# Performance work log

Measured on AMD Instinct MI355X. Metric: run time of the kernel, lower is better.

## Reference

```python
import jax, jax.numpy as jnp
import numpy as np

B, S, E, H = 1, 4096, 768, 12
D = E // H  # head_dim = 64


def setup_inputs() -> dict:
    key = jax.random.key(0)
    ks = jax.random.split(key, 6)
    scale = 0.02
    x = jax.random.normal(ks[0], (B, S, E), dtype=jnp.float32)
    Wq = jax.random.normal(ks[1], (E, E), dtype=jnp.float32) * scale
    Wk = jax.random.normal(ks[2], (E, E), dtype=jnp.float32) * scale
    Wv = jax.random.normal(ks[3], (E, E), dtype=jnp.float32) * scale
    Wo = jax.random.normal(ks[4], (E, E), dtype=jnp.float32) * scale
    bo = jax.random.normal(ks[5], (E,), dtype=jnp.float32) * scale
    mask = jnp.tril(jnp.ones((S, S), dtype=bool))[None, None]  # [1,1,S,S] causal
    return {"x": x, "Wq": Wq, "Wk": Wk, "Wv": Wv, "Wo": Wo, "bo": bo, "mask": mask}


def reference(x, Wq, Wk, Wv, Wo, bo, mask):
    # projections (torch Linear: y = x @ W.T; here W stored as [E,E] applied as x@W)
    q = jnp.einsum('bse,ef->bsf', x, Wq).reshape(B, S, H, D).transpose(0, 2, 1, 3)
    k = jnp.einsum('bse,ef->bsf', x, Wk).reshape(B, S, H, D).transpose(0, 2, 1, 3)
    v = jnp.einsum('bse,ef->bsf', x, Wv).reshape(B, S, H, D).transpose(0, 2, 1, 3)
    scores = jnp.einsum('bhqd,bhkd->bhqk', q, k) / jnp.sqrt(jnp.float32(D))
    scores = jnp.where(mask, scores, -jnp.inf)
    attn = jax.nn.softmax(scores, axis=-1)  # dropout p=0 -> identity
    ctx = jnp.einsum('bhqk,bhkd->bhqd', attn, v)
    ctx = ctx.transpose(0, 2, 1, 3).reshape(B, S, E)
    return jnp.einsum('bse,ef->bsf', ctx, Wo) + bo
```

## Files before the change

### kernel.cpp

```cpp
#include <hip/hip_runtime.h>
#include <math.h>

#define S 4096
#define E 768
#define H 12
#define Dh 64
#define SCALE2 0.1803368801111204f

typedef short short8 __attribute__((ext_vector_type(8)));
typedef float floatx4 __attribute__((ext_vector_type(4)));

__device__ __forceinline__ unsigned short f2bf(float f) {
    union { float f; unsigned int i; } c; c.f = f;
    unsigned int i = c.i;
    return (unsigned short)((i + 0x7fffu + ((i >> 16) & 1u)) >> 16);
}

__device__ __forceinline__ unsigned int pk_bf16(float lo, float hi) {
#if __has_builtin(__builtin_amdgcn_cvt_pk_bf16_f32)
    typedef __bf16 bf16x2 __attribute__((ext_vector_type(2)));
    union { bf16x2 v; unsigned int u; } c;
    c.v = __builtin_amdgcn_cvt_pk_bf16_f32(lo, hi);
    return c.u;
#else
    union { float f; unsigned int i; } a, b; a.f = lo; b.f = hi;
    return ((a.i + 0x8000u) >> 16) | ((b.i + 0x8000u) & 0xFFFF0000u);
#endif
}

__device__ __forceinline__ unsigned int scale_pk(unsigned int u, float s) {
    union { unsigned int i; float f; } lo, hi;
    lo.i = u << 16; hi.i = u & 0xffff0000u;
    return pk_bf16(lo.f * s, hi.f * s);
}

__device__ __forceinline__ void pk_atomic_add_bf16(unsigned short* addr, unsigned int bits) {
    unsigned long long a = (unsigned long long)addr;
    asm volatile("global_atomic_pk_add_bf16 %0, %1, off" :: "v"(a), "v"(bits) : "memory");
}

__device__ __forceinline__ void gload_lds16(const unsigned short* g, unsigned short* l) {
    __builtin_amdgcn_global_load_lds(
        (const __attribute__((address_space(1))) unsigned int*)g,
        (__attribute__((address_space(3))) unsigned int*)l, 16, 0, 0);
}

__global__ __launch_bounds__(256)
void prep_kernel(const float* __restrict__ x, unsigned short* __restrict__ xb,
                 const float* __restrict__ s0, const float* __restrict__ s1,
                 const float* __restrict__ s2, const float* __restrict__ s3,
                 unsigned short* __restrict__ d0, unsigned short* __restrict__ d1,
                 unsigned short* __restrict__ d2, unsigned short* __restrict__ d3,
                 char* __restrict__ zbase) {
    __shared__ unsigned short tile[32][33];
    const int b = blockIdx.x;
    const int tid = threadIdx.x;
    if (b < 2304) {
        int z = b / 576, rem = b - z * 576;
        int bx = rem % 24, by = rem / 24;
        const float* src = (z == 0) ? s0 : (z == 1) ? s1 : (z == 2) ? s2 : s3;
        unsigned short* dst = (z == 0) ? d0 : (z == 1) ? d1 : (z == 2) ? d2 : d3;
        int tx = tid & 31, ty = tid >> 5;
        int xcol = bx * 32 + tx;
        int y0 = by * 32;
        for (int j = ty; j < 32; j += 8)
            tile[j][tx] = f2bf(src[(size_t)(y0 + j) * E + xcol]);
        __syncthreads();
        int x2 = y0 + tx;
        int y2 = bx * 32;
        for (int j = ty; j < 32; j += 8)
            dst[(size_t)(y2 + j) * E + x2] = tile[tx][j];
    } else if (b < 3840) {
        int i = ((b - 2304) * 256 + tid) * 8;
        float4 f0 = *reinterpret_cast<const float4*>(x + i);
        float4 f1 = *reinterpret_cast<const float4*>(x + i + 4);
        unsigned short u[8];
        u[0]=f2bf(f0.x); u[1]=f2bf(f0.y); u[2]=f2bf(f0.z); u[3]=f2bf(f0.w);
        u[4]=f2bf(f1.x); u[5]=f2bf(f1.y); u[6]=f2bf(f1.z); u[7]=f2bf(f1.w);
        *reinterpret_cast<uint4*>(xb + i) = *reinterpret_cast<uint4*>(u);
    } else {
        size_t i = (size_t)(b - 3840) * 16384 + (size_t)tid * 64;
        uint4 z4 = make_uint4(0u, 0u, 0u, 0u);
        *reinterpret_cast<uint4*>(zbase + i)      = z4;
        *reinterpret_cast<uint4*>(zbase + i + 16) = z4;
        *reinterpret_cast<uint4*>(zbase + i + 32) = z4;
        *reinterpret_cast<uint4*>(zbase + i + 48) = z4;
    }
}

__global__ __launch_bounds__(256)
void gemm_qkv(const unsigned short* __restrict__ A,
              const unsigned short* __restrict__ BT,
              unsigned short* __restrict__ Qb, unsigned short* __restrict__ Kb,
              unsigned short* __restrict__ VTb) {
    __shared__ unsigned short Asm[128 * 64];
    __shared__ unsigned short Bsm[128 * 64];
    const int tid  = threadIdx.x;
    const int wave = tid >> 6, lane = tid & 63;
    const int quad = lane >> 4, l16 = lane & 15;
    const int lrow = lane >> 3, lchunk = lane & 7;
    const int bb = blockIdx.x;
    const int xcd = bb & 7, j = bb >> 3;
    const int mt = (xcd >> 1) * 8 + (j & 7);
    const int nt = (xcd & 1) * 9 + (j >> 3);
    const int n0 = nt * 128;
    const int m0 = mt * 128;
    const int aw = wave >> 1, bw = wave & 1;

    floatx4 acc[4][4];
    #pragma unroll
    for (int at = 0; at < 4; at++)
        #pragma unroll
        for (int ct = 0; ct < 4; ct++)
            #pragma unroll
            for (int r = 0; r < 4; r++) acc[at][ct][r] = 0.f;

    for (int k0 = 0; k0 < E; k0 += 64) {
        #pragma unroll
        for (int i = 0; i < 4; i++) {
            int rbase = wave * 32 + i * 8;
            int row   = rbase + lrow;
            int gc    = lchunk ^ (row & 7);
            gload_lds16(&A [(size_t)(m0 + row) * E + k0 + gc * 8], &Asm[rbase * 64]);
            gload_lds16(&BT[(size_t)(n0 + row) * E + k0 + gc * 8], &Bsm[rbase * 64]);
        }
        __syncthreads();
        #pragma unroll
        for (int kk = 0; kk < 2; kk++) {
            const int g = kk * 4 + quad;
            short8 af[4], bfr[4];
            #pragma unroll
            for (int t = 0; t < 4; t++) {
                int ar = aw * 64 + t * 16 + l16;
                af[t]  = *reinterpret_cast<const short8*>(&Asm[ar * 64 + (g ^ (ar & 7)) * 8]);
                int br = bw * 64 + t * 16 + l16;
                bfr[t] = *reinterpret_cast<const short8*>(&Bsm[br * 64 + (g ^ (br & 7)) * 8]);
            }
            #pragma unroll
            for (int at = 0; at < 4; at++)
                #pragma unroll
                for (int ct = 0; ct < 4; ct++)
                    acc[at][ct] = __builtin_amdgcn_mfma_f32_16x16x32_bf16(af[at], bfr[ct], acc[at][ct], 0, 0, 0);
        }
        __syncthreads();
    }

    const int sec = n0 / 768;
    const int nb  = n0 - sec * 768 + bw * 64;
    if (sec == 2) {
        #pragma unroll
        for (int at = 0; at < 4; at++)
            #pragma unroll
            for (int ct = 0; ct < 4; ct++) {
                int nsec = nb + ct * 16 + l16, hh = nsec >> 6, d = nsec & 63;
                int s0i = m0 + aw * 64 + at * 16 + quad * 4;
                uint2 w2;
                w2.x = pk_bf16(acc[at][ct][0], acc[at][ct][1]);
                w2.y = pk_bf16(acc[at][ct][2], acc[at][ct][3]);
                *reinterpret_cast<uint2*>(&VTb[(size_t)hh * Dh * S + (size_t)d * S + s0i]) = w2;
            }
    } else {
        #pragma unroll
        for (int at = 0; at < 4; at++)
            #pragma unroll
            for (int ct = 0; ct < 4; ct++) {
                int nsec = nb + ct * 16 + l16, hh = nsec >> 6, d = nsec & 63;
                #pragma unroll
                for (int r = 0; r < 4; r++) {
                    int s = m0 + aw * 64 + at * 16 + quad * 4 + r;
                    float v = acc[at][ct][r];
                    if (sec == 0) Qb[(size_t)hh * S * Dh + (size_t)s * Dh + d] = f2bf(v * SCALE2);
                    else          Kb[(size_t)hh * S * Dh + (size_t)s * Dh + d] = f2bf(v);
                }
            }
    }
}

__global__ __launch_bounds__(256)
void gemm_out(const unsigned short* __restrict__ ctxp,
              const unsigned short* __restrict__ BT,
              const float* __restrict__ lsumf,
              float* __restrict__ outp, const float* __restrict__ bias) {
    __shared__ unsigned short Asm[128 * 64];
    __shared__ unsigned short Bsm[64 * 64];
    const int tid  = threadIdx.x;
    const int wave = tid >> 6, lane = tid & 63;
    const int quad = lane >> 4, l16 = lane & 15;
    const int lrow = lane >> 3, lchunk = lane & 7;
    const int bb = blockIdx.x;
    const int xcd = bb & 7, j = bb >> 3;
    const int mt = (xcd >> 1) * 8 + (j & 7);
    const int nt = (xcd & 1) * 6 + (j >> 3);
    const int n0 = nt * 64;
    const int m0 = mt * 128;
    const int arow = tid >> 1, ahalf = tid & 1;

    floatx4 acc[2][4];
    #pragma unroll
    for (int at = 0; at < 2; at++)
        #pragma unroll
        for (int ct = 0; ct < 4; ct++)
            #pragma unroll
            for (int r = 0; r < 4; r++) acc[at][ct][r] = 0.f;

    for (int k0 = 0; k0 < E; k0 += 64) {
        {
            const unsigned short* asrc = ctxp + (size_t)(m0 + arow) * E + k0 + ahalf * 32;
            float linv = 1.0f / lsumf[(k0 >> 6) * S + m0 + arow];
            #pragma unroll
            for (int cc = 0; cc < 4; cc++) {
                uint4 u = *reinterpret_cast<const uint4*>(asrc + cc * 8);
                uint4 w;
                w.x = scale_pk(u.x, linv);
                w.y = scale_pk(u.y, linv);
                w.z = scale_pk(u.z, linv);
                w.w = scale_pk(u.w, linv);
                int chunk = ahalf * 4 + cc;
                *reinterpret_cast<uint4*>(&Asm[arow * 64 + (chunk ^ (arow & 7)) * 8]) = w;
            }
        }
        #pragma unroll
        for (int i = 0; i < 2; i++) {
            int rbase = wave * 16 + i * 8;
            int row   = rbase + lrow;
            int gc    = lchunk ^ (row & 7);
            gload_lds16(&BT[(size_t)(n0 + row) * E + k0 + gc * 8], &Bsm[rbase * 64]);
        }
        __syncthreads();
        #pragma unroll
        for (int kk = 0; kk < 2; kk++) {
            const int g = kk * 4 + quad;
            short8 af[2], bfr[4];
            #pragma unroll
            for (int t = 0; t < 2; t++) {
                int ar = wave * 32 + t * 16 + l16;
                af[t] = *reinterpret_cast<const short8*>(&Asm[ar * 64 + (g ^ (ar & 7)) * 8]);
            }
            #pragma unroll
            for (int ct = 0; ct < 4; ct++) {
                int br = ct * 16 + l16;
                bfr[ct] = *reinterpret_cast<const short8*>(&Bsm[br * 64 + (g ^ (br & 7)) * 8]);
            }
            #pragma unroll
            for (int at = 0; at < 2; at++)
                #pragma unroll
                for (int ct = 0; ct < 4; ct++)
                    acc[at][ct] = __builtin_amdgcn_mfma_f32_16x16x32_bf16(af[at], bfr[ct], acc[at][ct], 0, 0, 0);
        }
        __syncthreads();
    }

    #pragma unroll
    for (int at = 0; at < 2; at++)
        #pragma unroll
        for (int ct = 0; ct < 4; ct++) {
            int n = n0 + ct * 16 + l16;
            float bn = bias[n];
            #pragma unroll
            for (int r = 0; r < 4; r++) {
                int s = m0 + wave * 32 + at * 16 + quad * 4 + r;
                outp[(size_t)s * E + n] = acc[at][ct][r] + bn;
            }
        }
}

__global__ __launch_bounds__(256)
void attn_kernel(const unsigned short* __restrict__ Q,
                 const unsigned short* __restrict__ K,
                 const unsigned short* __restrict__ VT,
                 unsigned short* __restrict__ ctxp,
                 float* __restrict__ lsumf) {
    __shared__ unsigned short Ksm[2][64 * 64];
    __shared__ unsigned short Vsm[2][64 * 64];
    __shared__ unsigned short P[4][2][16 * 64];
    const int tid  = threadIdx.x;
    const int wave = tid >> 6, lane = tid & 63;
    const int quad = lane >> 4, l16 = lane & 15;
    const int lrow = lane >> 3, lchunk = lane & 7;

    const int b = blockIdx.x;
    const int w = b / H;
    const int h = b - w * H;
    int Qb, ck, nck;
    if (w < 32)       { Qb = 31 - (w >> 3);       ck = w & 7;         nck = 8; }
    else if (w < 60)  { int u = w - 32;  Qb = 27 - u / 7;  ck = u % 7; nck = 7; }
    else if (w < 84)  { int u = w - 60;  Qb = 23 - u / 6;  ck = u % 6; nck = 6; }
    else if (w < 104) { int u = w - 84;  Qb = 19 - u / 5;  ck = u % 5; nck = 5; }
    else if (w < 120) { int u = w - 104; Qb = 15 - (u >> 2); ck = u & 3; nck = 4; }
    else if (w < 132) { int u = w - 120; Qb = 11 - u / 3;  ck = u % 3; nck = 3; }
    else if (w < 140) { int u = w - 132; Qb = 7 - (u >> 1); ck = u & 1; nck = 2; }
    else              { Qb = 3 - (w - 140);       ck = 0;             nck = 1; }
    const int ntiles = 2 * Qb + 2;
    const int kt0 = (ntiles * ck) / nck;
    const int kt1 = (ntiles * (ck + 1)) / nck;

    const int qs = Qb * 128 + wave * 32;

    const unsigned short* Qh = Q  + (size_t)h * S * Dh;
    const unsigned short* Kh = K  + (size_t)h * S * Dh;
    const unsigned short* Vh = VT + (size_t)h * Dh * S;

    short8 bq[2][2];
    #pragma unroll
    for (int st = 0; st < 2; st++)
        #pragma unroll
        for (int c = 0; c < 2; c++)
            bq[st][c] = *reinterpret_cast<const short8*>(
                &Qh[(size_t)(qs + st * 16 + l16) * Dh + c * 32 + quad * 8]);

    float lsum[2] = {0.f, 0.f};
    floatx4 o[2][4];
    #pragma unroll
    for (int st = 0; st < 2; st++)
        #pragma unroll
        for (int ct = 0; ct < 4; ct++)
            #pragma unroll
            for (int r = 0; r < 4; r++) o[st][ct][r] = 0.f;

    auto stage = [&](int kt, int buf) {
        #pragma unroll
        for (int i = 0; i < 2; i++) {
            int rbase = wave * 16 + i * 8;
            int row   = rbase + lrow;
            int gc    = lchunk ^ (row & 7);
            gload_lds16(&Kh[(size_t)(kt * 64 + row) * Dh + gc * 8], &Ksm[buf][rbase * 64]);
            gload_lds16(&Vh[(size_t)row * S + kt * 64 + gc * 8],    &Vsm[buf][rbase * 64]);
        }
    };

    stage(kt0, 0);
    __syncthreads();

    for (int kt = kt0; kt < kt1; kt++) {
        const int cur = (kt - kt0) & 1;
        if (kt + 1 < kt1) stage(kt + 1, cur ^ 1);

        floatx4 sc[2][4];
        #pragma unroll
        for (int st = 0; st < 2; st++)
            #pragma unroll
            for (int ct = 0; ct < 4; ct++)
                #pragma unroll
                for (int r = 0; r < 4; r++) sc[st][ct][r] = 0.f;
        #pragma unroll
        for (int c = 0; c < 2; c++)
            #pragma unroll
            for (int ct = 0; ct < 4; ct++) {
                int kr = ct * 16 + l16;
                short8 ak = *reinterpret_cast<const short8*>(
                    &Ksm[cur][kr * 64 + ((c * 4 + quad) ^ (kr & 7)) * 8]);
                sc[0][ct] = __builtin_amdgcn_mfma_f32_16x16x32_bf16(ak, bq[0][c], sc[0][ct], 0, 0, 0);
                sc[1][ct] = __builtin_amdgcn_mfma_f32_16x16x32_bf16(ak, bq[1][c], sc[1][ct], 0, 0, 0);
            }

        if (kt >= 2 * Qb) {
            #pragma unroll
            for (int st = 0; st < 2; st++) {
                int qrow = qs + st * 16 + l16;
                #pragma unroll
                for (int ct = 0; ct < 4; ct++)
                    #pragma unroll
                    for (int r = 0; r < 4; r++) {
                        int kcol = kt * 64 + ct * 16 + quad * 4 + r;
                        if (kcol > qrow) sc[st][ct][r] = -INFINITY;
                    }
            }
        }

        #pragma unroll
        for (int st = 0; st < 2; st++)
            #pragma unroll
            for (int ct = 0; ct < 4; ct++) {
                float pv[4];
                #pragma unroll
                for (int r = 0; r < 4; r++) {
                    float p = __builtin_amdgcn_exp2f(sc[st][ct][r]);
                    lsum[st] += p;
                    pv[r] = p;
                }
                uint2 w2;
                w2.x = pk_bf16(pv[0], pv[1]);
                w2.y = pk_bf16(pv[2], pv[3]);
                int chunk = ct * 2 + (quad >> 1);
                int off = l16 * 64 + ((chunk ^ (l16 & 7)) * 8) + (quad & 1) * 4;
                *reinterpret_cast<uint2*>(&P[wave][st][off]) = w2;
            }
        __asm__ volatile("s_waitcnt lgkmcnt(0)" ::: "memory");

        #pragma unroll
        for (int c = 0; c < 2; c++) {
            short8 ap0 = *reinterpret_cast<const short8*>(
                &P[wave][0][l16 * 64 + (((c * 4 + quad) ^ (l16 & 7)) * 8)]);
            short8 ap1 = *reinterpret_cast<const short8*>(
                &P[wave][1][l16 * 64 + (((c * 4 + quad) ^ (l16 & 7)) * 8)]);
            #pragma unroll
            for (int ct = 0; ct < 4; ct++) {
                int vr = ct * 16 + l16;
                short8 bv = *reinterpret_cast<const short8*>(
                    &Vsm[cur][vr * 64 + ((c * 4 + quad) ^ (vr & 7)) * 8]);
                o[0][ct] = __builtin_amdgcn_mfma_f32_16x16x32_bf16(ap0, bv, o[0][ct], 0, 0, 0);
                o[1][ct] = __builtin_amdgcn_mfma_f32_16x16x32_bf16(ap1, bv, o[1][ct], 0, 0, 0);
            }
        }
        __syncthreads();
    }

    #pragma unroll
    for (int st = 0; st < 2; st++) {
        lsum[st] += __shfl_xor(lsum[st], 16, 64);
        lsum[st] += __shfl_xor(lsum[st], 32, 64);
    }
    if (quad == 0) {
        #pragma unroll
        for (int st = 0; st < 2; st++)
            atomicAdd(&lsumf[h * S + qs + st * 16 + l16], lsum[st]);
    }
    #pragma unroll
    for (int st = 0; st < 2; st++)
        #pragma unroll
        for (int r = 0; r < 4; r++) {
            int s = qs + st * 16 + quad * 4 + r;
            #pragma unroll
            for (int ct = 0; ct < 4; ct++) {
                float v  = o[st][ct][r];
                float vn = __shfl_xor(v, 1, 64);
                if ((l16 & 1) == 0)
                    pk_atomic_add_bf16(&ctxp[(size_t)s * E + h * Dh + ct * 16 + l16],
                                       pk_bf16(v, vn));
            }
        }
}

extern "C" void kernel_launch(void* const* d_in, const int* in_sizes, int n_in,
                              void* d_out, int out_size, void* d_ws, size_t ws_size,
                              hipStream_t stream) {
    const float* x  = (const float*)d_in[0];
    const float* Wq = (const float*)d_in[1];
    const float* Wk = (const float*)d_in[2];
    const float* Wv = (const float*)d_in[3];
    const float* Wo = (const float*)d_in[4];
    const float* bo = (const float*)d_in[5];
    float* out = (float*)d_out;

    char* ws = (char*)d_ws;
    const size_t WT = (size_t)E * E * 2;
    const size_t QB = (size_t)S * E * 2;
    unsigned short* WqT = (unsigned short*)(ws + 0 * WT);
    unsigned short* WkT = (unsigned short*)(ws + 1 * WT);
    unsigned short* WvT = (unsigned short*)(ws + 2 * WT);
    unsigned short* WoT = (unsigned short*)(ws + 3 * WT);
    unsigned short* xb  = (unsigned short*)(ws + 4 * WT + 0 * QB);
    unsigned short* Qbf = (unsigned short*)(ws + 4 * WT + 1 * QB);
    unsigned short* Kbf = (unsigned short*)(ws + 4 * WT + 2 * QB);
    unsigned short* VTb = (unsigned short*)(ws + 4 * WT + 3 * QB);
    unsigned short* ctxp  = (unsigned short*)(ws + 4 * WT + 4 * QB);
    float*          lsumf = (float*)(ws + 4 * WT + 5 * QB);

    prep_kernel<<<4236, 256, 0, stream>>>(
        x, xb, Wq, Wk, Wv, Wo, WqT, WkT, WvT, WoT, (char*)ctxp);

    gemm_qkv<<<576, 256, 0, stream>>>(xb, WqT, Qbf, Kbf, VTb);

    attn_kernel<<<1728, 256, 0, stream>>>(Qbf, Kbf, VTb, ctxp, lsumf);

    gemm_out<<<384, 256, 0, stream>>>(ctxp, WoT, lsumf, out, bo);
}
```

Before: 244.4 us.

## Keep softmax probabilities in registers, use fp16 MFMA for PV

The attention kernel stops writing the exponentiated scores to shared memory and reading them back. The score accumulator layout is fed directly as the B operand of a 16x16x16 fp16 MFMA, with V (now stored as fp16) supplying the A operand, so the output tile comes out transposed. The V projection epilogue switches to fp16 round-toward-zero packing, and the final context write uses packed bf16 atomics without cross-lane shuffles. The aim is to remove the LDS round trip and its wait on the P tile, at the cost of using the half-K MFMA shape (twice as many MFMA instructions) and fp16 range and precision for P and V.

```diff
diff --git a/kernel.cpp b/kernel.cpp
--- a/kernel.cpp
+++ b/kernel.cpp
@@ -9,6 +9,8 @@
 
 typedef short short8 __attribute__((ext_vector_type(8)));
 typedef float floatx4 __attribute__((ext_vector_type(4)));
+typedef __fp16 half4 __attribute__((ext_vector_type(4)));
+typedef __fp16 half2n __attribute__((ext_vector_type(2)));
 
 __device__ __forceinline__ unsigned short f2bf(float f) {
     union { float f; unsigned int i; } c; c.f = f;
@@ -26,6 +28,12 @@
     union { float f; unsigned int i; } a, b; a.f = lo; b.f = hi;
     return ((a.i + 0x8000u) >> 16) | ((b.i + 0x8000u) & 0xFFFF0000u);
 #endif
+}
+
+__device__ __forceinline__ unsigned int pk_f16(float lo, float hi) {
+    union { half2n h; unsigned int u; } c;
+    c.h = __builtin_amdgcn_cvt_pkrtz(lo, hi);
+    return c.u;
 }
 
 __device__ __forceinline__ unsigned int scale_pk(unsigned int u, float s) {
@@ -155,8 +163,8 @@
                 int nsec = nb + ct * 16 + l16, hh = nsec >> 6, d = nsec & 63;
                 int s0i = m0 + aw * 64 + at * 16 + quad * 4;
                 uint2 w2;
-                w2.x = pk_bf16(acc[at][ct][0], acc[at][ct][1]);
-                w2.y = pk_bf16(acc[at][ct][2], acc[at][ct][3]);
+                w2.x = pk_f16(acc[at][ct][0], acc[at][ct][1]);
+                w2.y = pk_f16(acc[at][ct][2], acc[at][ct][3]);
                 *reinterpret_cast<uint2*>(&VTb[(size_t)hh * Dh * S + (size_t)d * S + s0i]) = w2;
             }
     } else {
@@ -272,7 +280,6 @@
                  float* __restrict__ lsumf) {
     __shared__ unsigned short Ksm[2][64 * 64];
     __shared__ unsigned short Vsm[2][64 * 64];
-    __shared__ unsigned short P[4][2][16 * 64];
     const int tid  = threadIdx.x;
     const int wave = tid >> 6, lane = tid & 63;
     const int quad = lane >> 4, l16 = lane & 15;
@@ -313,9 +320,9 @@
     #pragma unroll
     for (int st = 0; st < 2; st++)
         #pragma unroll
-        for (int ct = 0; ct < 4; ct++)
-            #pragma unroll
-            for (int r = 0; r < 4; r++) o[st][ct][r] = 0.f;
+        for (int dt = 0; dt < 4; dt++)
+            #pragma unroll
+            for (int r = 0; r < 4; r++) o[st][dt][r] = 0.f;
 
     auto stage = [&](int kt, int buf) {
         #pragma unroll
@@ -367,6 +374,7 @@
             }
         }
 
+        half4 pb[2][4];
         #pragma unroll
         for (int st = 0; st < 2; st++)
             #pragma unroll
@@ -378,28 +386,23 @@
                     lsum[st] += p;
                     pv[r] = p;
                 }
-                uint2 w2;
-                w2.x = pk_bf16(pv[0], pv[1]);
-                w2.y = pk_bf16(pv[2], pv[3]);
-                int chunk = ct * 2 + (quad >> 1);
-                int off = l16 * 64 + ((chunk ^ (l16 & 7)) * 8) + (quad & 1) * 4;
-                *reinterpret_cast<uint2*>(&P[wave][st][off]) = w2;
-            }
-        __asm__ volatile("s_waitcnt lgkmcnt(0)" ::: "memory");
-
-        #pragma unroll
-        for (int c = 0; c < 2; c++) {
-            short8 ap0 = *reinterpret_cast<const short8*>(
-                &P[wave][0][l16 * 64 + (((c * 4 + quad) ^ (l16 & 7)) * 8)]);
-            short8 ap1 = *reinterpret_cast<const short8*>(
-                &P[wave][1][l16 * 64 + (((c * 4 + quad) ^ (l16 & 7)) * 8)]);
-            #pragma unroll
-            for (int ct = 0; ct < 4; ct++) {
-                int vr = ct * 16 + l16;
-                short8 bv = *reinterpret_cast<const short8*>(
-                    &Vsm[cur][vr * 64 + ((c * 4 + quad) ^ (vr & 7)) * 8]);
-                o[0][ct] = __builtin_amdgcn_mfma_f32_16x16x32_bf16(ap0, bv, o[0][ct], 0, 0, 0);
-                o[1][ct] = __builtin_amdgcn_mfma_f32_16x16x32_bf16(ap1, bv, o[1][ct], 0, 0, 0);
+                half2n lo = __builtin_amdgcn_cvt_pkrtz(pv[0], pv[1]);
+                half2n hi = __builtin_amdgcn_cvt_pkrtz(pv[2], pv[3]);
+                half4 hb;
+                hb[0] = lo[0]; hb[1] = lo[1]; hb[2] = hi[0]; hb[3] = hi[1];
+                pb[st][ct] = hb;
+            }
+
+        #pragma unroll
+        for (int dt = 0; dt < 4; dt++) {
+            int vrow = dt * 16 + l16;
+            #pragma unroll
+            for (int ct = 0; ct < 4; ct++) {
+                int swch = (ct * 2 + (quad >> 1)) ^ (vrow & 7);
+                half4 av = *reinterpret_cast<const half4*>(
+                    &Vsm[cur][vrow * 64 + swch * 8 + (quad & 1) * 4]);
+                o[0][dt] = __builtin_amdgcn_mfma_f32_16x16x16f16(av, pb[0][ct], o[0][dt], 0, 0, 0);
+                o[1][dt] = __builtin_amdgcn_mfma_f32_16x16x16f16(av, pb[1][ct], o[1][dt], 0, 0, 0);
             }
         }
         __syncthreads();
@@ -416,19 +419,17 @@
             atomicAdd(&lsumf[h * S + qs + st * 16 + l16], lsum[st]);
     }
     #pragma unroll
-    for (int st = 0; st < 2; st++)
-        #pragma unroll
-        for (int r = 0; r < 4; r++) {
-            int s = qs + st * 16 + quad * 4 + r;
-            #pragma unroll
-            for (int ct = 0; ct < 4; ct++) {
-                float v  = o[st][ct][r];
-                float vn = __shfl_xor(v, 1, 64);
-                if ((l16 & 1) == 0)
-                    pk_atomic_add_bf16(&ctxp[(size_t)s * E + h * Dh + ct * 16 + l16],
-                                       pk_bf16(v, vn));
-            }
-        }
+    for (int st = 0; st < 2; st++) {
+        int s = qs + st * 16 + l16;
+        #pragma unroll
+        for (int dt = 0; dt < 4; dt++) {
+            int d0 = dt * 16 + quad * 4;
+            pk_atomic_add_bf16(&ctxp[(size_t)s * E + h * Dh + d0],
+                               pk_bf16(o[st][dt][0], o[st][dt][1]));
+            pk_atomic_add_bf16(&ctxp[(size_t)s * E + h * Dh + d0 + 2],
+                               pk_bf16(o[st][dt][2], o[st][dt][3]));
+        }
+    }
 }
 
 extern "C" void kernel_launch(void* const* d_in, const int* in_sizes, int n_in,
```

New measurement: 275.3 us. 1.13x slower.
